# Kernel optimization log

Hardware: AMD Instinct MI355X
Metric: run time of the kernel (lower is better)

## Reference

```python
import jax, jax.numpy as jnp
import numpy as np

NB = 5  # frequency bands


def _ln(x, g, b, eps=1e-5):
    m = jnp.mean(x, axis=-1, keepdims=True)
    v = jnp.var(x, axis=-1, keepdims=True)
    return (x - m) / jnp.sqrt(v + eps) * g + b


def _graph_adj(x, adj_w, sw1, sb1, sw2, sb2, pos_factor, pos_enc):
    # x: [B, D, N] -> degree-normalized adjacency [B, N, N]
    d = x.shape[1]
    xt = jnp.swapaxes(x, 1, 2)  # [B, N, D]
    # concat-MLP first layer split: cat(xi, xj) @ W1 == xi @ W1[:d] + xj @ W1[d:]
    a = xt @ sw1[:d]
    bpart = xt @ sw1[d:]
    h = jax.nn.elu(a[:, :, None, :] + bpart[:, None, :, :] + sb1)  # [B, N, N, H]
    dyn = jax.nn.sigmoid(jnp.squeeze(h @ sw2, -1) + sb2)  # [B, N, N]
    static = jax.nn.softmax(adj_w, axis=-1)
    pos = jax.nn.softmax(pos_enc, axis=-1)
    comb = jax.nn.softmax(static + dyn + pos_factor * pos, axis=-1)
    deg = jnp.sum(comb, axis=-1)
    dis = (deg + 1e-8) ** -0.5
    return dis[:, :, None] * comb * dis[:, None, :]


def _gcn(x, adj, w, b):
    # x: [B, D, N], adj: [B, N, N] -> [B, D_out, N]
    xt = jnp.swapaxes(x, 1, 2)
    out = jnp.einsum('bij,bjd->bid', adj, xt) @ w + b
    return jnp.swapaxes(out, 1, 2)


def _mha(x, qkv_w, qkv_b, ow, ob, nh=4):
    B, S, D = x.shape
    dh = D // nh
    q, k, v = jnp.split(x @ qkv_w + qkv_b, 3, axis=-1)
    q = q.reshape(B, S, nh, dh)
    k = k.reshape(B, S, nh, dh)
    v = v.reshape(B, S, nh, dh)
    att = jax.nn.softmax(jnp.einsum('bihd,bjhd->bhij', q, k) / float(np.sqrt(dh)), axis=-1)
    o = jnp.einsum('bhij,bjhd->bihd', att, v).reshape(B, S, D)
    return o @ ow + ob


def setup_inputs():
    key = jax.random.key(0)
    B, D, N = 16, 256, 64
    ks = iter(jax.random.split(key, 40))

    def rn(shape, s=0.05):
        return jax.random.normal(next(ks), shape, dtype=jnp.float32) * s

    eyeN = jnp.eye(N, dtype=jnp.float32)
    return dict(
        feature=jax.random.normal(next(ks), (B, NB * D, 1, N), dtype=jnp.float32),
        l_adj_w=jnp.tile(eyeN[None], (NB, 1, 1)),
        l_sim_w1=rn((NB, 2 * D, D)), l_sim_b1=jnp.zeros((NB, D), jnp.float32),
        l_sim_w2=rn((NB, D, 1)), l_sim_b2=jnp.zeros((NB, 1), jnp.float32),
        l_pos_factor=jnp.full((NB,), 0.5, jnp.float32),
        l_pos_enc=jnp.tile(eyeN[None], (NB, 1, 1)),
        l_gcn_w=rn((NB, D, D)), l_gcn_b=jnp.zeros((NB, D), jnp.float32),
        g_adj_w=jnp.eye(NB, dtype=jnp.float32),
        g_sim_w1=rn((2 * D, D)), g_sim_b1=jnp.zeros((D,), jnp.float32),
        g_sim_w2=rn((D, 1)), g_sim_b2=jnp.zeros((1,), jnp.float32),
        g_pos_factor=jnp.float32(0.5),
        g_pos_enc=jnp.eye(NB, dtype=jnp.float32),
        g_gcn_w=rn((D, D)), g_gcn_b=jnp.zeros((D,), jnp.float32),
        qkv_w=rn((D, 3 * D)), qkv_b=jnp.zeros((3 * D,), jnp.float32),
        attn_ow=rn((D, D)), attn_ob=jnp.zeros((D,), jnp.float32),
        ln1_g=jnp.ones((D,), jnp.float32), ln1_b=jnp.zeros((D,), jnp.float32),
        ln2_g=jnp.ones((D,), jnp.float32), ln2_b=jnp.zeros((D,), jnp.float32),
        mlp_w1=rn((D, 4 * D)), mlp_b1=jnp.zeros((4 * D,), jnp.float32),
        mlp_w2=rn((4 * D, D)), mlp_b2=jnp.zeros((D,), jnp.float32),
        imp_w=rn((NB, N, 1)), imp_b=jnp.zeros((NB, 1), jnp.float32),
    )


def reference(feature, l_adj_w, l_sim_w1, l_sim_b1, l_sim_w2, l_sim_b2,
              l_pos_factor, l_pos_enc, l_gcn_w, l_gcn_b,
              g_adj_w, g_sim_w1, g_sim_b1, g_sim_w2, g_sim_b2,
              g_pos_factor, g_pos_enc, g_gcn_w, g_gcn_b,
              qkv_w, qkv_b, attn_ow, attn_ob,
              ln1_g, ln1_b, ln2_g, ln2_b,
              mlp_w1, mlp_b1, mlp_w2, mlp_b2,
              imp_w, imp_b):
    B = feature.shape[0]
    D = l_gcn_w.shape[-1]
    N = feature.shape[-1]
    # [B, 5*D, 1, N] -> [5, B, D, N] band-major
    x5 = jnp.moveaxis(feature.reshape(B, NB, D, N), 1, 0)
    # per-band local graphs + GCNs (vmapped over the 5 bands)
    local_adj = jax.vmap(_graph_adj)(x5, l_adj_w, l_sim_w1, l_sim_b1,
                                     l_sim_w2, l_sim_b2, l_pos_factor, l_pos_enc)
    local_out = jax.vmap(_gcn)(x5, local_adj, l_gcn_w, l_gcn_b)  # [5, B, D, N]
    scale_nodes = jnp.moveaxis(jnp.mean(local_out, axis=-1), 0, 1)  # [B, 5, D]
    # cross-band attention block (pre: MHA + residual + LN, then MLP + residual + LN)
    attn = _mha(scale_nodes, qkv_w, qkv_b, attn_ow, attn_ob)
    h1 = _ln(scale_nodes + attn, ln1_g, ln1_b)
    mlp = jax.nn.gelu(h1 @ mlp_w1 + mlp_b1, approximate=False) @ mlp_w2 + mlp_b2
    se = _ln(h1 + mlp, ln2_g, ln2_b)  # [B, 5, D]
    # global scale graph over the 5 band nodes
    xg = jnp.swapaxes(se, 1, 2)  # [B, D, 5]
    g_adj = _graph_adj(xg, g_adj_w, g_sim_w1, g_sim_b1, g_sim_w2, g_sim_b2,
                       g_pos_factor, g_pos_enc)
    g_out = jnp.swapaxes(_gcn(xg, g_adj, g_gcn_w, g_gcn_b), 1, 2)  # [B, 5, D]
    # modulate each local band feature by its global scale vector
    enh = local_out * jnp.moveaxis(g_out, 1, 0)[..., None]  # [5, B, D, N]
    # per-band importance projection over channels: [5, B, D, 1]
    out5 = jnp.einsum('kbdn,kno->kbdo', enh, imp_w) + imp_b[:, None, None, :]
    output = jnp.moveaxis(out5, 0, 1).reshape(B, NB * D, 1, 1)
    return output, g_adj, jnp.moveaxis(local_out, 0, 1)
```

## Files before the change

kernel.cpp:

```cpp
#include <hip/hip_runtime.h>
#include <hip/hip_bf16.h>

#define NBANDS 5
#define BATCH  16
#define DIM    256
#define NNODE  64
#define SEQ    5
#define NHEAD  4
#define DHEAD  64

typedef __hip_bfloat16 bf16;
typedef unsigned short ushort_t;
typedef __attribute__((ext_vector_type(8))) short short8;
typedef __attribute__((ext_vector_type(4))) float float4v;

__device__ __forceinline__ float bu2f(ushort_t u){
    bf16 h = *reinterpret_cast<bf16*>(&u);
    return __bfloat162float(h);
}
__device__ __forceinline__ ushort_t f2bu(float x){
    bf16 h = __float2bfloat16(x);
    return *reinterpret_cast<ushort_t*>(&h);
}

__global__ void __launch_bounds__(256) k_head(
    const float* __restrict__ l_adj_w, const float* __restrict__ l_pos_enc,
    const float* __restrict__ l_pf,
    const float* __restrict__ g_adj_w, const float* __restrict__ g_pos_enc,
    const float* __restrict__ g_pf,
    float* __restrict__ sbase, float* __restrict__ gbase,
    const float* __restrict__ w1, const float* __restrict__ gw,
    ushort_t* __restrict__ w1bt, ushort_t* __restrict__ gwbt,
    const float* __restrict__ feat,
    ushort_t* __restrict__ xtb, ushort_t* __restrict__ xtT)
{
    int blk = blockIdx.x;
    int tid = threadIdx.x;
    __shared__ ushort_t tile[64][65];

    if (blk < 80) {
        int r = blk*4 + (tid>>6);
        int k = r >> 6, i = r & 63;
        int t = tid & 63;
        float aw = l_adj_w[(k*NNODE + i)*NNODE + t];
        float pe = l_pos_enc[(k*NNODE + i)*NNODE + t];
        float m1 = aw, m2 = pe;
        for (int o=32;o>0;o>>=1){ m1 = fmaxf(m1, __shfl_xor(m1,o,64)); m2 = fmaxf(m2, __shfl_xor(m2,o,64)); }
        float e1 = __expf(aw-m1), e2 = __expf(pe-m2);
        float s1=e1, s2=e2;
        for (int o=32;o>0;o>>=1){ s1 += __shfl_xor(s1,o,64); s2 += __shfl_xor(s2,o,64); }
        float pf = l_pf[k];
        sbase[(k*NNODE+i)*NNODE + t] = e1/s1 + pf*(e2/s2);
    } else if (blk == 80) {
        if (tid < NBANDS) {
            int i = tid;
            float r1[NBANDS], r2[NBANDS];
            float m1=-1e30f, m2=-1e30f;
            for (int j=0;j<NBANDS;j++){
                r1[j]=g_adj_w[i*NBANDS+j]; r2[j]=g_pos_enc[i*NBANDS+j];
                m1=fmaxf(m1,r1[j]); m2=fmaxf(m2,r2[j]);
            }
            float s1=0.f,s2=0.f;
            for (int j=0;j<NBANDS;j++){ r1[j]=__expf(r1[j]-m1); r2[j]=__expf(r2[j]-m2); s1+=r1[j]; s2+=r2[j]; }
            float pf = g_pf[0];
            for (int j=0;j<NBANDS;j++) gbase[i*NBANDS+j] = r1[j]/s1 + pf*(r2[j]/s2);
        }
    } else if (blk < 321) {
        int idx = blk - 81;
        int inst = idx >> 4;
        int t = idx & 15;
        int r0 = (t>>2)*64, c0 = (t&3)*64;
        const float* src; ushort_t* dst;
        if (inst < 10){
            int k = inst>>1, half = inst&1;
            src = w1  + ((size_t)k*512 + half*256)*256;
            dst = w1bt+ ((size_t)k*512 + half*256)*256;
        } else {
            int k = inst-10;
            src = gw  + (size_t)k*65536;
            dst = gwbt+ (size_t)k*65536;
        }
        int jj = tid & 63, i4 = tid >> 6;
        for (int p=0;p<16;p++){
            int i = p*4 + i4;
            tile[i][jj] = f2bu(src[(size_t)(r0+i)*256 + c0 + jj]);
        }
        __syncthreads();
        for (int p=0;p<16;p++){
            int i = p*4 + i4;
            dst[(size_t)(c0+i)*256 + r0 + jj] = tile[jj][i];
        }
    } else {
        int idx = blk - 321;
        int k = idx >> 6;
        int b = (idx >> 2) & 15;
        int dt = idx & 3;
        const float* src = feat + ((size_t)b*NBANDS*DIM + (size_t)k*DIM)*NNODE;
        ushort_t* dst = xtb + (size_t)(k*BATCH+b)*NNODE*DIM;
        ushort_t* dstT = xtT + (size_t)(k*BATCH+b)*DIM*NNODE;
        for (int u=0; u<16; ++u){
            int i = dt*4096 + u*256 + tid;
            dstT[i] = f2bu(src[i]);
        }
        for (int r=0;r<16;r++){
            int dp = r*4 + (tid>>6);
            int n  = tid & 63;
            tile[dp][n] = f2bu(src[(size_t)(dt*64+dp)*NNODE + n]);
        }
        __syncthreads();
        for (int r=0;r<16;r++){
            int n  = r*4 + (tid>>6);
            int dp = tid & 63;
            dst[(size_t)n*DIM + dt*64 + dp] = tile[dp][n];
        }
    }
}

__global__ void __launch_bounds__(256) k_ab_mfma(const ushort_t* __restrict__ xtb,
                        const ushort_t* __restrict__ w1bt, const float* __restrict__ b1,
                        ushort_t* __restrict__ aab, ushort_t* __restrict__ bbb)
{
    int blk = blockIdx.x;
    int kband = blk / (BATCH*8);
    int b = (blk/8) % BATCH;
    int nblk = blk & 7;
    int tid = threadIdx.x;
    int wave = tid>>6, lane = tid&63;
    int c16 = lane & 15, quad = lane >> 4;
    int m0 = wave*16;
    size_t rowbase = (size_t)(kband*BATCH+b)*NNODE;
    const ushort_t* Aptr = xtb + (rowbase + m0 + c16)*DIM + quad*8;
    const ushort_t* Bbase = w1bt + (size_t)kband*512*DIM;
    int ncol0 = nblk*64;
    const ushort_t* Bptr0 = Bbase + (size_t)(ncol0 +  0 + c16)*DIM + quad*8;
    const ushort_t* Bptr1 = Bbase + (size_t)(ncol0 + 16 + c16)*DIM + quad*8;
    const ushort_t* Bptr2 = Bbase + (size_t)(ncol0 + 32 + c16)*DIM + quad*8;
    const ushort_t* Bptr3 = Bbase + (size_t)(ncol0 + 48 + c16)*DIM + quad*8;
    float4v acc0 = {0.f,0.f,0.f,0.f}, acc1 = acc0, acc2 = acc0, acc3 = acc0;
    #pragma unroll
    for (int ks=0; ks<8; ++ks){
        short8 a  = *reinterpret_cast<const short8*>(Aptr  + ks*32);
        short8 b0 = *reinterpret_cast<const short8*>(Bptr0 + ks*32);
        short8 b1v= *reinterpret_cast<const short8*>(Bptr1 + ks*32);
        short8 b2 = *reinterpret_cast<const short8*>(Bptr2 + ks*32);
        short8 b3 = *reinterpret_cast<const short8*>(Bptr3 + ks*32);
        acc0 = __builtin_amdgcn_mfma_f32_16x16x32_bf16(a, b0, acc0, 0,0,0);
        acc1 = __builtin_amdgcn_mfma_f32_16x16x32_bf16(a, b1v, acc1, 0,0,0);
        acc2 = __builtin_amdgcn_mfma_f32_16x16x32_bf16(a, b2, acc2, 0,0,0);
        acc3 = __builtin_amdgcn_mfma_f32_16x16x32_bf16(a, b3, acc3, 0,0,0);
    }
    int half = nblk >> 2;
    int cbase = (nblk & 3)*64;
    ushort_t* dst = half ? bbb : aab;
    float4v accs[4] = {acc0, acc1, acc2, acc3};
    #pragma unroll
    for (int nt=0; nt<4; ++nt){
        int cg = cbase + nt*16 + c16;
        float bias = half ? 0.f : b1[kband*DIM + cg];
        #pragma unroll
        for (int r=0;r<4;r++){
            int m = m0 + quad*4 + r;
            dst[(rowbase + m)*DIM + cg] = f2bu(accs[nt][r] + bias);
        }
    }
}

__global__ void __launch_bounds__(256) k_dyn_comb(const ushort_t* __restrict__ aab,
                           const ushort_t* __restrict__ bbb,
                           const float* __restrict__ w2, const float* __restrict__ b2arr,
                           const float* __restrict__ sbase,
                           ushort_t* __restrict__ combb)
{
    int blk = blockIdx.x;
    int k = blk / (BATCH*16);
    int b = (blk / 16) % BATCH;
    int i0 = (blk % 16) * 4;
    int kb = k*BATCH + b;
    __shared__ ushort_t bs[64][260];
    __shared__ float arows[4][DIM];
    __shared__ float w2s[DIM];
    int tid = threadIdx.x;
    int wave = tid >> 6, lane = tid & 63;
    const ushort_t* bsrc = bbb + (size_t)kb*NNODE*DIM;
    for (int u=0; u<16; ++u){
        int idx = u*1024 + tid*4;
        int row = idx >> 8, col = idx & 255;
        *reinterpret_cast<ushort4*>(&bs[row][col]) =
            *reinterpret_cast<const ushort4*>(&bsrc[(size_t)row*DIM + col]);
    }
    for (int r=0;r<4;r++) arows[r][tid] = bu2f(aab[((size_t)kb*NNODE + i0 + r)*DIM + tid]);
    w2s[tid] = w2[k*DIM + tid];
    __syncthreads();

    int i = i0 + wave;
    float acc = 0.f;
    #pragma unroll 4
    for (int dd=0; dd<64; ++dd){
        ushort4 bv = *reinterpret_cast<const ushort4*>(&bs[lane][dd*4]);
        float4 av = *reinterpret_cast<const float4*>(&arows[wave][dd*4]);
        float4 wv = *reinterpret_cast<const float4*>(&w2s[dd*4]);
        float v0 = av.x + bu2f(bv.x);
        float v1 = av.y + bu2f(bv.y);
        float v2 = av.z + bu2f(bv.z);
        float v3 = av.w + bu2f(bv.w);
        float e0 = (v0>0.f)? v0 : (__expf(v0)-1.f);
        float e1 = (v1>0.f)? v1 : (__expf(v1)-1.f);
        float e2 = (v2>0.f)? v2 : (__expf(v2)-1.f);
        float e3 = (v3>0.f)? v3 : (__expf(v3)-1.f);
        acc += e0*wv.x + e1*wv.y + e2*wv.z + e3*wv.w;
    }
    float sb2 = b2arr[k];
    float sg = 1.f/(1.f + __expf(-(acc + sb2)));
    float val = sbase[(k*NNODE + i)*NNODE + lane] + sg;
    float m = val;
    for (int o=32;o>0;o>>=1) m = fmaxf(m, __shfl_xor(m,o,64));
    float e = __expf(val - m);
    float s = e;
    for (int o=32;o>0;o>>=1) s += __shfl_xor(s,o,64);
    combb[((size_t)kb*NNODE + i)*NNODE + lane] = f2bu(e/s);
}

__global__ void __launch_bounds__(256) k_y_mfma(const ushort_t* __restrict__ combb,
                       const ushort_t* __restrict__ xtT,
                       ushort_t* __restrict__ yb)
{
    int blk = blockIdx.x;
    int kband = blk / (BATCH*4);
    int b = (blk/4) % BATCH;
    int nblk = blk & 3;
    int tid = threadIdx.x;
    int wave = tid>>6, lane = tid&63;
    int c16 = lane & 15, quad = lane >> 4;
    int m0 = wave*16;
    int kb = kband*BATCH + b;
    const ushort_t* Aptr = combb + ((size_t)kb*NNODE + m0 + c16)*NNODE + quad*8;
    const ushort_t* Bbase = xtT + (size_t)kb*DIM*NNODE;
    int ncol0 = nblk*64;
    const ushort_t* Bptr0 = Bbase + (size_t)(ncol0 +  0 + c16)*NNODE + quad*8;
    const ushort_t* Bptr1 = Bbase + (size_t)(ncol0 + 16 + c16)*NNODE + quad*8;
    const ushort_t* Bptr2 = Bbase + (size_t)(ncol0 + 32 + c16)*NNODE + quad*8;
    const ushort_t* Bptr3 = Bbase + (size_t)(ncol0 + 48 + c16)*NNODE + quad*8;
    float4v acc0 = {0.f,0.f,0.f,0.f}, acc1 = acc0, acc2 = acc0, acc3 = acc0;
    #pragma unroll
    for (int ks=0; ks<2; ++ks){
        short8 a  = *reinterpret_cast<const short8*>(Aptr  + ks*32);
        short8 b0 = *reinterpret_cast<const short8*>(Bptr0 + ks*32);
        short8 b1v= *reinterpret_cast<const short8*>(Bptr1 + ks*32);
        short8 b2 = *reinterpret_cast<const short8*>(Bptr2 + ks*32);
        short8 b3 = *reinterpret_cast<const short8*>(Bptr3 + ks*32);
        acc0 = __builtin_amdgcn_mfma_f32_16x16x32_bf16(a, b0, acc0, 0,0,0);
        acc1 = __builtin_amdgcn_mfma_f32_16x16x32_bf16(a, b1v, acc1, 0,0,0);
        acc2 = __builtin_amdgcn_mfma_f32_16x16x32_bf16(a, b2, acc2, 0,0,0);
        acc3 = __builtin_amdgcn_mfma_f32_16x16x32_bf16(a, b3, acc3, 0,0,0);
    }
    size_t rowbase = (size_t)kb*NNODE;
    float4v accs[4] = {acc0, acc1, acc2, acc3};
    #pragma unroll
    for (int nt=0; nt<4; ++nt){
        int cg = ncol0 + nt*16 + c16;
        #pragma unroll
        for (int r=0;r<4;r++){
            int m = m0 + quad*4 + r;
            yb[(rowbase + m)*DIM + cg] = f2bu(accs[nt][r]);
        }
    }
}

__global__ void __launch_bounds__(256) k_gcn_mfma(const ushort_t* __restrict__ yb,
                         const ushort_t* __restrict__ gwbt, const float* __restrict__ gb,
                         const float* __restrict__ imp_w,
                         float* __restrict__ out_local,
                         float* __restrict__ scalew, float* __restrict__ impw)
{
    int blk = blockIdx.x;
    int kband = blk / (BATCH*4);
    int b = (blk/4) % BATCH;
    int nblk = blk & 3;
    int tid = threadIdx.x;
    int wave = tid>>6, lane = tid&63;
    int c16 = lane & 15, quad = lane >> 4;
    int m0 = wave*16;
    int kb = kband*BATCH + b;
    __shared__ float iw_s[NNODE];
    __shared__ float sred[4][64];
    __shared__ float ired[4][64];
    if (tid < NNODE) iw_s[tid] = imp_w[kband*NNODE + tid];
    const ushort_t* Aptr = yb + ((size_t)kb*NNODE + m0 + c16)*DIM + quad*8;
    const ushort_t* Bbase = gwbt + (size_t)kband*DIM*DIM;
    int ncol0 = nblk*64;
    const ushort_t* Bptr0 = Bbase + (size_t)(ncol0 +  0 + c16)*DIM + quad*8;
    const ushort_t* Bptr1 = Bbase + (size_t)(ncol0 + 16 + c16)*DIM + quad*8;
    const ushort_t* Bptr2 = Bbase + (size_t)(ncol0 + 32 + c16)*DIM + quad*8;
    const ushort_t* Bptr3 = Bbase + (size_t)(ncol0 + 48 + c16)*DIM + quad*8;
    float4v acc0 = {0.f,0.f,0.f,0.f}, acc1 = acc0, acc2 = acc0, acc3 = acc0;
    #pragma unroll
    for (int ks=0; ks<8; ++ks){
        short8 a  = *reinterpret_cast<const short8*>(Aptr  + ks*32);
        short8 b0 = *reinterpret_cast<const short8*>(Bptr0 + ks*32);
        short8 b1v= *reinterpret_cast<const short8*>(Bptr1 + ks*32);
        short8 b2 = *reinterpret_cast<const short8*>(Bptr2 + ks*32);
        short8 b3 = *reinterpret_cast<const short8*>(Bptr3 + ks*32);
        acc0 = __builtin_amdgcn_mfma_f32_16x16x32_bf16(a, b0, acc0, 0,0,0);
        acc1 = __builtin_amdgcn_mfma_f32_16x16x32_bf16(a, b1v, acc1, 0,0,0);
        acc2 = __builtin_amdgcn_mfma_f32_16x16x32_bf16(a, b2, acc2, 0,0,0);
        acc3 = __builtin_amdgcn_mfma_f32_16x16x32_bf16(a, b3, acc3, 0,0,0);
    }
    __syncthreads();
    float4v accs[4] = {acc0, acc1, acc2, acc3};
    #pragma unroll
    for (int nt=0; nt<4; ++nt){
        int cg = ncol0 + nt*16 + c16;
        float bias = gb[kband*DIM + cg];
        float v0 = accs[nt][0]+bias, v1 = accs[nt][1]+bias, v2 = accs[nt][2]+bias, v3 = accs[nt][3]+bias;
        float4 v = make_float4(v0, v1, v2, v3);
        float* dst = out_local + ((size_t)(b*NBANDS + kband)*DIM + cg)*NNODE + m0 + quad*4;
        *reinterpret_cast<float4*>(dst) = v;
        int nb = m0 + quad*4;
        float s  = v0 + v1 + v2 + v3;
        float di = v0*iw_s[nb] + v1*iw_s[nb+1] + v2*iw_s[nb+2] + v3*iw_s[nb+3];
        s  += __shfl_xor(s, 16, 64);  s  += __shfl_xor(s, 32, 64);
        di += __shfl_xor(di, 16, 64); di += __shfl_xor(di, 32, 64);
        if (quad == 0){
            sred[wave][nt*16 + c16] = s;
            ired[wave][nt*16 + c16] = di;
        }
    }
    __syncthreads();
    if (tid < 64){
        float s  = sred[0][tid] + sred[1][tid] + sred[2][tid] + sred[3][tid];
        float di = ired[0][tid] + ired[1][tid] + ired[2][tid] + ired[3][tid];
        size_t o = ((size_t)b*SEQ + kband)*DIM + ncol0 + tid;
        scalew[o] = s * (1.f/64.f);
        impw[o]   = di;
    }
}

template<int COLS, int SLICES>
__global__ void __launch_bounds__(256) k_gemv(const float* __restrict__ x, const float* __restrict__ w,
                       const float* __restrict__ bias, float* __restrict__ out,
                       int K, int N, int act)
{
    int chunks = N / COLS;
    int row = blockIdx.x / chunks;
    int n0 = (blockIdx.x % chunks) * COLS;
    int c = threadIdx.x % COLS, s = threadIdx.x / COLS;
    __shared__ float xs[1024];
    __shared__ float part[SLICES][COLS];
    for (int i = threadIdx.x; i < K; i += 256) xs[i] = x[(size_t)row*K + i];
    __syncthreads();
    int klen = K / SLICES;
    const float* wp = w + (size_t)(s*klen)*N + n0 + c;
    const float* xp = xs + s*klen;
    float acc = 0.f;
    #pragma unroll 8
    for (int i = 0; i < klen; ++i) acc += xp[i] * wp[(size_t)i*N];
    part[s][c] = acc;
    __syncthreads();
    if (s == 0){
        float v = bias[n0+c];
        #pragma unroll
        for (int q=0;q<SLICES;q++) v += part[q][c];
        if (act) v = 0.5f*v*(1.f + erff(v*0.70710678118654752f));
        out[(size_t)row*N + n0 + c] = v;
    }
}

__global__ void __launch_bounds__(256) k_projattn(const float* __restrict__ qkvw,
                        const float* __restrict__ ow, const float* __restrict__ ob,
                        float* __restrict__ projw)
{
    int row = blockIdx.x / 4;
    int n0 = (blockIdx.x % 4) * 64;
    int b = row / SEQ, i = row % SEQ;
    int tid = threadIdx.x;
    int h = tid >> 6, l = tid & 63;
    __shared__ float xs[DIM];
    __shared__ float part[4][64];
    const float* base = qkvw + (size_t)b*SEQ*3*DIM;
    float qv = base[(size_t)i*3*DIM + h*DHEAD + l];
    float pj[SEQ];
    #pragma unroll
    for (int j=0;j<SEQ;j++){
        float p = qv * base[(size_t)j*3*DIM + DIM + h*DHEAD + l];
        for (int o=32;o>0;o>>=1) p += __shfl_xor(p,o,64);
        pj[j] = p * 0.125f;
    }
    float m = pj[0];
    #pragma unroll
    for (int j=1;j<SEQ;j++) m = fmaxf(m, pj[j]);
    float ssum = 0.f;
    #pragma unroll
    for (int j=0;j<SEQ;j++){ pj[j] = __expf(pj[j]-m); ssum += pj[j]; }
    float inv = 1.f/ssum;
    float o = 0.f;
    #pragma unroll
    for (int j=0;j<SEQ;j++) o += pj[j]*inv * base[(size_t)j*3*DIM + 2*DIM + h*DHEAD + l];
    xs[tid] = o;
    __syncthreads();
    int c = tid & 63, s = tid >> 6;
    const float* wp = ow + (size_t)(s*64)*DIM + n0 + c;
    const float* xp = xs + s*64;
    float acc = 0.f;
    #pragma unroll 8
    for (int k=0;k<64;++k) acc += xp[k] * wp[(size_t)k*DIM];
    part[s][c] = acc;
    __syncthreads();
    if (s == 0){
        projw[(size_t)row*DIM + n0 + c] = ob[n0+c] + part[0][c]+part[1][c]+part[2][c]+part[3][c];
    }
}

__device__ __forceinline__ float block_ln(float v, int tid, float* red, float g, float bln)
{
    float s = v;
    for (int o=32;o>0;o>>=1) s += __shfl_xor(s,o,64);
    int wave = tid>>6, lane = tid&63;
    if (lane==0) red[wave] = s;
    __syncthreads();
    float mean = (red[0]+red[1]+red[2]+red[3]) * (1.f/DIM);
    float c = v - mean;
    float q = c*c;
    for (int o=32;o>0;o>>=1) q += __shfl_xor(q,o,64);
    __syncthreads();
    if (lane==0) red[wave] = q;
    __syncthreads();
    float var = (red[0]+red[1]+red[2]+red[3]) * (1.f/DIM);
    return c * rsqrtf(var + 1e-5f) * g + bln;
}

__global__ void __launch_bounds__(256) k_mlp1_ln(const float* __restrict__ projw,
                         const float* __restrict__ scalew,
                         const float* __restrict__ ln1_g, const float* __restrict__ ln1_b,
                         const float* __restrict__ w1, const float* __restrict__ b1,
                         float* __restrict__ h1w, float* __restrict__ mhw)
{
    int row = blockIdx.x / 16;
    int n0 = (blockIdx.x % 16) * 64;
    int tid = threadIdx.x;
    __shared__ float xs[DIM];
    __shared__ float red[4];
    __shared__ float part[4][64];
    float v = projw[(size_t)row*DIM + tid] + scalew[(size_t)row*DIM + tid];
    float h = block_ln(v, tid, red, ln1_g[tid], ln1_b[tid]);
    xs[tid] = h;
    if ((blockIdx.x % 16) == 0) h1w[(size_t)row*DIM + tid] = h;
    __syncthreads();
    int c = tid & 63, s = tid >> 6;
    const float* wp = w1 + (size_t)(s*64)*1024 + n0 + c;
    const float* xp = xs + s*64;
    float acc = 0.f;
    #pragma unroll 8
    for (int i=0;i<64;++i) acc += xp[i] * wp[(size_t)i*1024];
    part[s][c] = acc;
    __syncthreads();
    if (s == 0){
        float o = b1[n0+c] + part[0][c] + part[1][c] + part[2][c] + part[3][c];
        o = 0.5f*o*(1.f + erff(o*0.70710678118654752f));
        mhw[(size_t)row*1024 + n0 + c] = o;
    }
}

__global__ void __launch_bounds__(256) k_gab_ln(const float* __restrict__ m2w,
                        const float* __restrict__ h1w,
                        const float* __restrict__ ln2_g, const float* __restrict__ ln2_b,
                        const float* __restrict__ gw1, const float* __restrict__ gb1,
                        float* __restrict__ sew, float* __restrict__ gaw, float* __restrict__ gbw)
{
    int row = blockIdx.x / 4;
    int n0 = (blockIdx.x % 4) * 64;
    int tid = threadIdx.x;
    __shared__ float xs[DIM];
    __shared__ float red[4];
    __shared__ float partA[4][64];
    __shared__ float partB[4][64];
    float v = m2w[(size_t)row*DIM + tid] + h1w[(size_t)row*DIM + tid];
    float h = block_ln(v, tid, red, ln2_g[tid], ln2_b[tid]);
    xs[tid] = h;
    if ((blockIdx.x % 4) == 0) sew[(size_t)row*DIM + tid] = h;
    __syncthreads();
    int c = tid & 63, s = tid >> 6;
    const float* wpA = gw1 + (size_t)(s*64)*DIM + n0 + c;
    const float* wpB = wpA + (size_t)DIM*DIM;
    const float* xp = xs + s*64;
    float aA = 0.f, aB = 0.f;
    #pragma unroll 8
    for (int i=0;i<64;++i){
        float xv = xp[i];
        aA += xv * wpA[(size_t)i*DIM];
        aB += xv * wpB[(size_t)i*DIM];
    }
    partA[s][c] = aA;
    partB[s][c] = aB;
    __syncthreads();
    if (s == 0){
        gaw[(size_t)row*DIM + n0 + c] = gb1[n0+c] + partA[0][c]+partA[1][c]+partA[2][c]+partA[3][c];
        gbw[(size_t)row*DIM + n0 + c] = partB[0][c]+partB[1][c]+partB[2][c]+partB[3][c];
    }
}

__global__ void __launch_bounds__(256) k_goutfin(const float* __restrict__ gaw,
                        const float* __restrict__ gbw,
                        const float* __restrict__ gw2, const float* __restrict__ gb2,
                        const float* __restrict__ gbase,
                        const float* __restrict__ sew,
                        const float* __restrict__ ggw, const float* __restrict__ ggb,
                        const float* __restrict__ impw, const float* __restrict__ imp_b,
                        float* __restrict__ out0, float* __restrict__ out_gadj)
{
    int row = blockIdx.x / 4;
    int n0 = (blockIdx.x % 4) * 64;
    int b = row / SEQ, i = row % SEQ;
    int tid = threadIdx.x;
    int wave = tid >> 6, lane = tid & 63;
    __shared__ float dyn_s[SEQ];
    __shared__ float xs[DIM];
    __shared__ float part[4][64];
    for (int j = wave; j < SEQ; j += 4){
        const float* gar = gaw + (size_t)row*DIM;
        const float* gbr = gbw + ((size_t)b*SEQ + j)*DIM;
        float acc = 0.f;
        #pragma unroll
        for (int m=0;m<4;m++){
            int dd = lane + m*64;
            float v = gar[dd] + gbr[dd];
            float e = (v>0.f) ? v : (__expf(v)-1.f);
            acc += e * gw2[dd];
        }
        for (int o=32;o>0;o>>=1) acc += __shfl_xor(acc,o,64);
        if (lane==0) dyn_s[j] = acc;
    }
    __syncthreads();
    float gc[SEQ];
    {
        float sb2 = gb2[0];
        float m = -1e30f;
        #pragma unroll
        for (int j=0;j<SEQ;j++){
            float sg = 1.f/(1.f+__expf(-(dyn_s[j]+sb2)));
            gc[j] = gbase[i*SEQ+j] + sg;
            m = fmaxf(m, gc[j]);
        }
        float ssum=0.f;
        #pragma unroll
        for (int j=0;j<SEQ;j++){ gc[j]=__expf(gc[j]-m); ssum+=gc[j]; }
        float inv = 1.f/ssum;
        #pragma unroll
        for (int j=0;j<SEQ;j++) gc[j] *= inv;
    }
    if (n0 == 0 && tid < SEQ) out_gadj[((size_t)b*SEQ+i)*SEQ + tid] = gc[tid];
    float t = 0.f;
    #pragma unroll
    for (int j=0;j<SEQ;j++) t += gc[j]*sew[((size_t)b*SEQ + j)*DIM + tid];
    xs[tid] = t;
    __syncthreads();
    int c = tid & 63, s = tid >> 6;
    const float* wp = ggw + (size_t)(s*64)*DIM + n0 + c;
    const float* xp = xs + s*64;
    float acc = 0.f;
    #pragma unroll 8
    for (int k=0;k<64;++k) acc += xp[k] * wp[(size_t)k*DIM];
    part[s][c] = acc;
    __syncthreads();
    if (s == 0){
        float g = ggb[n0+c] + part[0][c]+part[1][c]+part[2][c]+part[3][c];
        size_t o = (size_t)row*DIM + n0 + c;
        out0[o] = g * impw[o] + imp_b[i];
    }
}

extern "C" void kernel_launch(void* const* d_in, const int* in_sizes, int n_in,
                              void* d_out, int out_size, void* d_ws, size_t ws_size,
                              hipStream_t stream)
{
    const float* feature      = (const float*)d_in[0];
    const float* l_adj_w      = (const float*)d_in[1];
    const float* l_sim_w1     = (const float*)d_in[2];
    const float* l_sim_b1     = (const float*)d_in[3];
    const float* l_sim_w2     = (const float*)d_in[4];
    const float* l_sim_b2     = (const float*)d_in[5];
    const float* l_pos_factor = (const float*)d_in[6];
    const float* l_pos_enc    = (const float*)d_in[7];
    const float* l_gcn_w      = (const float*)d_in[8];
    const float* l_gcn_b      = (const float*)d_in[9];
    const float* g_adj_w      = (const float*)d_in[10];
    const float* g_sim_w1     = (const float*)d_in[11];
    const float* g_sim_b1     = (const float*)d_in[12];
    const float* g_sim_w2     = (const float*)d_in[13];
    const float* g_sim_b2     = (const float*)d_in[14];
    const float* g_pos_factor = (const float*)d_in[15];
    const float* g_pos_enc    = (const float*)d_in[16];
    const float* g_gcn_w      = (const float*)d_in[17];
    const float* g_gcn_b      = (const float*)d_in[18];
    const float* qkv_w        = (const float*)d_in[19];
    const float* qkv_b        = (const float*)d_in[20];
    const float* attn_ow      = (const float*)d_in[21];
    const float* attn_ob      = (const float*)d_in[22];
    const float* ln1_g        = (const float*)d_in[23];
    const float* ln1_b        = (const float*)d_in[24];
    const float* ln2_g        = (const float*)d_in[25];
    const float* ln2_b        = (const float*)d_in[26];
    const float* mlp_w1       = (const float*)d_in[27];
    const float* mlp_b1       = (const float*)d_in[28];
    const float* mlp_w2       = (const float*)d_in[29];
    const float* mlp_b2       = (const float*)d_in[30];
    const float* imp_w        = (const float*)d_in[31];
    const float* imp_b        = (const float*)d_in[32];

    float* out0      = (float*)d_out;
    float* out_gadj  = out0 + (size_t)BATCH*NBANDS*DIM;
    float* out_local = out_gadj + (size_t)BATCH*NBANDS*NBANDS;

    const size_t BIG = (size_t)NBANDS*BATCH*NNODE*DIM;
    ushort_t* xtb   = (ushort_t*)d_ws;
    ushort_t* aab   = xtb + BIG;
    ushort_t* bbb   = aab + BIG;
    ushort_t* xtT   = bbb + BIG;
    ushort_t* yb    = aab;
    ushort_t* w1bt  = xtT + BIG;
    ushort_t* gwbt  = w1bt + (size_t)NBANDS*512*DIM;
    ushort_t* combb = gwbt + (size_t)NBANDS*DIM*DIM;
    float* fp = (float*)(combb + (size_t)NBANDS*BATCH*NNODE*NNODE);
    float* sbase  = fp; fp += NBANDS*NNODE*NNODE;
    float* gbase  = fp; fp += 32;
    float* scalew = fp; fp += BATCH*SEQ*DIM;
    float* impw   = fp; fp += BATCH*SEQ*DIM;
    float* qkvw   = fp; fp += BATCH*SEQ*3*DIM;
    float* projw  = fp; fp += BATCH*SEQ*DIM;
    float* h1w    = fp; fp += BATCH*SEQ*DIM;
    float* mhw    = fp; fp += BATCH*SEQ*4*DIM;
    float* m2w    = fp; fp += BATCH*SEQ*DIM;
    float* sew    = fp; fp += BATCH*SEQ*DIM;
    float* gaw    = fp; fp += BATCH*SEQ*DIM;
    float* gbw    = fp; fp += BATCH*SEQ*DIM;

    const int ROWS = BATCH*SEQ;

    k_head<<<641, 256, 0, stream>>>(l_adj_w, l_pos_enc, l_pos_factor,
                                    g_adj_w, g_pos_enc, g_pos_factor,
                                    sbase, gbase,
                                    l_sim_w1, l_gcn_w, w1bt, gwbt,
                                    feature, xtb, xtT);
    k_ab_mfma<<<NBANDS*BATCH*8, 256, 0, stream>>>(xtb, w1bt, l_sim_b1, aab, bbb);
    k_dyn_comb<<<NBANDS*BATCH*16, 256, 0, stream>>>(aab, bbb, l_sim_w2, l_sim_b2, sbase, combb);
    k_y_mfma<<<NBANDS*BATCH*4, 256, 0, stream>>>(combb, xtT, yb);
    k_gcn_mfma<<<NBANDS*BATCH*4, 256, 0, stream>>>(yb, gwbt, l_gcn_b, imp_w,
                                                   out_local, scalew, impw);
    k_gemv<64,4><<<ROWS*12, 256, 0, stream>>>(scalew, qkv_w, qkv_b, qkvw, 256, 768, 0);
    k_projattn<<<ROWS*4, 256, 0, stream>>>(qkvw, attn_ow, attn_ob, projw);
    k_mlp1_ln<<<ROWS*16, 256, 0, stream>>>(projw, scalew, ln1_g, ln1_b, mlp_w1, mlp_b1, h1w, mhw);
    k_gemv<32,8><<<ROWS*8, 256, 0, stream>>>(mhw, mlp_w2, mlp_b2, m2w, 1024, 256, 0);
    k_gab_ln<<<ROWS*4, 256, 0, stream>>>(m2w, h1w, ln2_g, ln2_b, g_sim_w1, g_sim_b1, sew, gaw, gbw);
    k_goutfin<<<ROWS*4, 256, 0, stream>>>(gaw, gbw, g_sim_w2, g_sim_b2, gbase,
                                          sew, g_gcn_w, g_gcn_b, impw, imp_b,
                                          out0, out_gadj);
}
```

Before: 218.8 us.

## Fuse local graph pipeline into one kernel and tail into per-batch kernel

Replaces the chain of local-graph kernels (feature transpose, A/B projection, dynamic adjacency, Y, GCN) with one kernel per (band, batch, 16-row quarter) that keeps features, projections, adjacency rows and Y in shared memory. The six small attention/MLP/global-graph kernels become a single 1024-thread kernel per batch. This removes many launches and the large bf16 intermediate round-trips through global memory. In exchange, each block recomputes the full B projection for all 64 nodes (four times redundantly across quarters), and the tail runs on only 16 blocks, so parallelism in the tail is low.

```diff
diff --git a/kernel.cpp b/kernel.cpp
--- a/kernel.cpp
+++ b/kernel.cpp
@@ -6,14 +6,14 @@
 #define DIM    256
 #define NNODE  64
 #define SEQ    5
-#define NHEAD  4
-#define DHEAD  64
 
 typedef __hip_bfloat16 bf16;
 typedef unsigned short ushort_t;
 typedef __attribute__((ext_vector_type(8))) short short8;
 typedef __attribute__((ext_vector_type(4))) float float4v;
 
+#define MFMA __builtin_amdgcn_mfma_f32_16x16x32_bf16
+
 __device__ __forceinline__ float bu2f(ushort_t u){
     bf16 h = *reinterpret_cast<bf16*>(&u);
     return __bfloat162float(h);
@@ -21,6 +21,9 @@
 __device__ __forceinline__ ushort_t f2bu(float x){
     bf16 h = __float2bfloat16(x);
     return *reinterpret_cast<ushort_t*>(&h);
+}
+__device__ __forceinline__ float elu(float v){
+    return (v > 0.f) ? v : (__expf(v) - 1.f);
 }
 
 __global__ void __launch_bounds__(256) k_head(
@@ -30,9 +33,7 @@
     const float* __restrict__ g_pf,
     float* __restrict__ sbase, float* __restrict__ gbase,
     const float* __restrict__ w1, const float* __restrict__ gw,
-    ushort_t* __restrict__ w1bt, ushort_t* __restrict__ gwbt,
-    const float* __restrict__ feat,
-    ushort_t* __restrict__ xtb, ushort_t* __restrict__ xtT)
+    ushort_t* __restrict__ w1bt, ushort_t* __restrict__ gwbt)
 {
     int blk = blockIdx.x;
     int tid = threadIdx.x;
@@ -65,7 +66,7 @@
             float pf = g_pf[0];
             for (int j=0;j<NBANDS;j++) gbase[i*NBANDS+j] = r1[j]/s1 + pf*(r2[j]/s2);
         }
-    } else if (blk < 321) {
+    } else {
         int idx = blk - 81;
         int inst = idx >> 4;
         int t = idx & 15;
@@ -90,481 +91,483 @@
             int i = p*4 + i4;
             dst[(size_t)(c0+i)*256 + r0 + jj] = tile[jj][i];
         }
-    } else {
-        int idx = blk - 321;
-        int k = idx >> 6;
-        int b = (idx >> 2) & 15;
-        int dt = idx & 3;
-        const float* src = feat + ((size_t)b*NBANDS*DIM + (size_t)k*DIM)*NNODE;
-        ushort_t* dst = xtb + (size_t)(k*BATCH+b)*NNODE*DIM;
-        ushort_t* dstT = xtT + (size_t)(k*BATCH+b)*DIM*NNODE;
-        for (int u=0; u<16; ++u){
-            int i = dt*4096 + u*256 + tid;
-            dstT[i] = f2bu(src[i]);
-        }
-        for (int r=0;r<16;r++){
-            int dp = r*4 + (tid>>6);
-            int n  = tid & 63;
-            tile[dp][n] = f2bu(src[(size_t)(dt*64+dp)*NNODE + n]);
-        }
-        __syncthreads();
-        for (int r=0;r<16;r++){
-            int n  = r*4 + (tid>>6);
-            int dp = tid & 63;
-            dst[(size_t)n*DIM + dt*64 + dp] = tile[dp][n];
-        }
-    }
-}
-
-__global__ void __launch_bounds__(256) k_ab_mfma(const ushort_t* __restrict__ xtb,
-                        const ushort_t* __restrict__ w1bt, const float* __restrict__ b1,
-                        ushort_t* __restrict__ aab, ushort_t* __restrict__ bbb)
+    }
+}
+
+__global__ void __launch_bounds__(512) k_graph(
+    const float* __restrict__ feat,
+    const ushort_t* __restrict__ w1bt, const float* __restrict__ b1,
+    const float* __restrict__ w2, const float* __restrict__ b2arr,
+    const float* __restrict__ sbase,
+    const ushort_t* __restrict__ gwbt, const float* __restrict__ gb,
+    const float* __restrict__ imp_w,
+    float* __restrict__ out_local,
+    float* __restrict__ scalew4, float* __restrict__ impw4)
 {
-    int blk = blockIdx.x;
-    int kband = blk / (BATCH*8);
-    int b = (blk/8) % BATCH;
-    int nblk = blk & 7;
+    int k  = blockIdx.x >> 6;
+    int b  = (blockIdx.x >> 2) & 15;
+    int iq = blockIdx.x & 3;
+    int i0 = iq << 4;
     int tid = threadIdx.x;
-    int wave = tid>>6, lane = tid&63;
-    int c16 = lane & 15, quad = lane >> 4;
-    int m0 = wave*16;
-    size_t rowbase = (size_t)(kband*BATCH+b)*NNODE;
-    const ushort_t* Aptr = xtb + (rowbase + m0 + c16)*DIM + quad*8;
-    const ushort_t* Bbase = w1bt + (size_t)kband*512*DIM;
-    int ncol0 = nblk*64;
-    const ushort_t* Bptr0 = Bbase + (size_t)(ncol0 +  0 + c16)*DIM + quad*8;
-    const ushort_t* Bptr1 = Bbase + (size_t)(ncol0 + 16 + c16)*DIM + quad*8;
-    const ushort_t* Bptr2 = Bbase + (size_t)(ncol0 + 32 + c16)*DIM + quad*8;
-    const ushort_t* Bptr3 = Bbase + (size_t)(ncol0 + 48 + c16)*DIM + quad*8;
-    float4v acc0 = {0.f,0.f,0.f,0.f}, acc1 = acc0, acc2 = acc0, acc3 = acc0;
+    int w = tid >> 6, lane = tid & 63, c16 = lane & 15, quad = lane >> 4;
+
+    __shared__ union {
+        ushort_t xtb[64][264];
+        ushort_t ab[80][264];
+    } U;
+    __shared__ ushort_t cs[16][72];
+    __shared__ ushort_t ys[16][264];
+    __shared__ float w2s[DIM];
+
+    const float* src = feat + ((size_t)b*NBANDS + k)*DIM*NNODE;
+
+    if (tid < DIM) w2s[tid] = w2[k*DIM + tid];
     #pragma unroll
-    for (int ks=0; ks<8; ++ks){
-        short8 a  = *reinterpret_cast<const short8*>(Aptr  + ks*32);
-        short8 b0 = *reinterpret_cast<const short8*>(Bptr0 + ks*32);
-        short8 b1v= *reinterpret_cast<const short8*>(Bptr1 + ks*32);
-        short8 b2 = *reinterpret_cast<const short8*>(Bptr2 + ks*32);
-        short8 b3 = *reinterpret_cast<const short8*>(Bptr3 + ks*32);
-        acc0 = __builtin_amdgcn_mfma_f32_16x16x32_bf16(a, b0, acc0, 0,0,0);
-        acc1 = __builtin_amdgcn_mfma_f32_16x16x32_bf16(a, b1v, acc1, 0,0,0);
-        acc2 = __builtin_amdgcn_mfma_f32_16x16x32_bf16(a, b2, acc2, 0,0,0);
-        acc3 = __builtin_amdgcn_mfma_f32_16x16x32_bf16(a, b3, acc3, 0,0,0);
-    }
-    int half = nblk >> 2;
-    int cbase = (nblk & 3)*64;
-    ushort_t* dst = half ? bbb : aab;
-    float4v accs[4] = {acc0, acc1, acc2, acc3};
+    for (int u = 0; u < 32; ++u){
+        int idx = u*512 + tid;
+        U.xtb[idx & 63][idx >> 6] = f2bu(src[idx]);
+    }
+    __syncthreads();
+
+    int col0 = w*32 + c16;
+    int col1 = col0 + 16;
+
+    const ushort_t* Ba = w1bt + (size_t)k*512*DIM;
+    const ushort_t* Bb = Ba + 256*DIM;
+    float4v z = {0.f,0.f,0.f,0.f};
+    float4v aA0=z, aA1=z;
+    float4v aB00=z,aB01=z,aB10=z,aB11=z,aB20=z,aB21=z,aB30=z,aB31=z;
     #pragma unroll
-    for (int nt=0; nt<4; ++nt){
-        int cg = cbase + nt*16 + c16;
-        float bias = half ? 0.f : b1[kband*DIM + cg];
-        #pragma unroll
-        for (int r=0;r<4;r++){
-            int m = m0 + quad*4 + r;
-            dst[(rowbase + m)*DIM + cg] = f2bu(accs[nt][r] + bias);
-        }
-    }
-}
-
-__global__ void __launch_bounds__(256) k_dyn_comb(const ushort_t* __restrict__ aab,
-                           const ushort_t* __restrict__ bbb,
-                           const float* __restrict__ w2, const float* __restrict__ b2arr,
-                           const float* __restrict__ sbase,
-                           ushort_t* __restrict__ combb)
+    for (int ks = 0; ks < 8; ++ks){
+        int ko = ks*32 + quad*8;
+        short8 fa = *reinterpret_cast<const short8*>(&U.xtb[i0 + c16][ko]);
+        short8 f0 = *reinterpret_cast<const short8*>(&U.xtb[ 0 + c16][ko]);
+        short8 f1 = *reinterpret_cast<const short8*>(&U.xtb[16 + c16][ko]);
+        short8 f2 = *reinterpret_cast<const short8*>(&U.xtb[32 + c16][ko]);
+        short8 f3 = *reinterpret_cast<const short8*>(&U.xtb[48 + c16][ko]);
+        short8 wa0 = *reinterpret_cast<const short8*>(Ba + (size_t)col0*DIM + ko);
+        short8 wa1 = *reinterpret_cast<const short8*>(Ba + (size_t)col1*DIM + ko);
+        short8 wb0 = *reinterpret_cast<const short8*>(Bb + (size_t)col0*DIM + ko);
+        short8 wb1 = *reinterpret_cast<const short8*>(Bb + (size_t)col1*DIM + ko);
+        aA0  = MFMA(fa, wa0, aA0, 0,0,0);
+        aA1  = MFMA(fa, wa1, aA1, 0,0,0);
+        aB00 = MFMA(f0, wb0, aB00, 0,0,0);
+        aB01 = MFMA(f0, wb1, aB01, 0,0,0);
+        aB10 = MFMA(f1, wb0, aB10, 0,0,0);
+        aB11 = MFMA(f1, wb1, aB11, 0,0,0);
+        aB20 = MFMA(f2, wb0, aB20, 0,0,0);
+        aB21 = MFMA(f2, wb1, aB21, 0,0,0);
+        aB30 = MFMA(f3, wb0, aB30, 0,0,0);
+        aB31 = MFMA(f3, wb1, aB31, 0,0,0);
+    }
+    __syncthreads();
+    {
+        float bias0 = b1[k*DIM + col0];
+        float bias1 = b1[k*DIM + col1];
+        int r0 = quad*4;
+        #pragma unroll
+        for (int r = 0; r < 4; ++r){
+            U.ab[r0 + r][col0]      = f2bu(aA0[r] + bias0);
+            U.ab[r0 + r][col1]      = f2bu(aA1[r] + bias1);
+            U.ab[16 + r0 + r][col0] = f2bu(aB00[r]);
+            U.ab[16 + r0 + r][col1] = f2bu(aB01[r]);
+            U.ab[32 + r0 + r][col0] = f2bu(aB10[r]);
+            U.ab[32 + r0 + r][col1] = f2bu(aB11[r]);
+            U.ab[48 + r0 + r][col0] = f2bu(aB20[r]);
+            U.ab[48 + r0 + r][col1] = f2bu(aB21[r]);
+            U.ab[64 + r0 + r][col0] = f2bu(aB30[r]);
+            U.ab[64 + r0 + r][col1] = f2bu(aB31[r]);
+        }
+    }
+    __syncthreads();
+
+    {
+        int il0 = w*2, il1 = w*2 + 1;
+        float acc0 = 0.f, acc1 = 0.f;
+        const ushort_t* ar0 = U.ab[il0];
+        const ushort_t* ar1 = U.ab[il1];
+        const ushort_t* br  = U.ab[16 + lane];
+        #pragma unroll 4
+        for (int dd = 0; dd < 64; ++dd){
+            ushort4 bv = *reinterpret_cast<const ushort4*>(br  + dd*4);
+            ushort4 a0 = *reinterpret_cast<const ushort4*>(ar0 + dd*4);
+            ushort4 a1 = *reinterpret_cast<const ushort4*>(ar1 + dd*4);
+            float4 wv  = *reinterpret_cast<const float4*>(&w2s[dd*4]);
+            float bx = bu2f(bv.x), by = bu2f(bv.y), bz = bu2f(bv.z), bq = bu2f(bv.w);
+            acc0 += elu(bu2f(a0.x)+bx)*wv.x + elu(bu2f(a0.y)+by)*wv.y
+                  + elu(bu2f(a0.z)+bz)*wv.z + elu(bu2f(a0.w)+bq)*wv.w;
+            acc1 += elu(bu2f(a1.x)+bx)*wv.x + elu(bu2f(a1.y)+by)*wv.y
+                  + elu(bu2f(a1.z)+bz)*wv.z + elu(bu2f(a1.w)+bq)*wv.w;
+        }
+        float sb2 = b2arr[k];
+        float sg0 = 1.f/(1.f + __expf(-(acc0 + sb2)));
+        float sg1 = 1.f/(1.f + __expf(-(acc1 + sb2)));
+        float val0 = sbase[(k*NNODE + i0 + il0)*NNODE + lane] + sg0;
+        float val1 = sbase[(k*NNODE + i0 + il1)*NNODE + lane] + sg1;
+        float m0 = val0, m1 = val1;
+        for (int o=32;o>0;o>>=1){ m0 = fmaxf(m0, __shfl_xor(m0,o,64)); m1 = fmaxf(m1, __shfl_xor(m1,o,64)); }
+        float e0 = __expf(val0 - m0), e1 = __expf(val1 - m1);
+        float s0 = e0, s1 = e1;
+        for (int o=32;o>0;o>>=1){ s0 += __shfl_xor(s0,o,64); s1 += __shfl_xor(s1,o,64); }
+        cs[il0][lane] = f2bu(e0/s0);
+        cs[il1][lane] = f2bu(e1/s1);
+    }
+    __syncthreads();
+
+    {
+        float4v aY0 = z, aY1 = z;
+        #pragma unroll
+        for (int ks = 0; ks < 2; ++ks){
+            int ko = ks*32 + quad*8;
+            short8 af = *reinterpret_cast<const short8*>(&cs[c16][ko]);
+            const float* f0p = src + (size_t)col0*NNODE + ko;
+            const float* f1p = src + (size_t)col1*NNODE + ko;
+            float4 x0 = *reinterpret_cast<const float4*>(f0p);
+            float4 x1 = *reinterpret_cast<const float4*>(f0p+4);
+            float4 y0 = *reinterpret_cast<const float4*>(f1p);
+            float4 y1 = *reinterpret_cast<const float4*>(f1p+4);
+            short8 bf0, bf1;
+            bf0[0]=(short)f2bu(x0.x); bf0[1]=(short)f2bu(x0.y); bf0[2]=(short)f2bu(x0.z); bf0[3]=(short)f2bu(x0.w);
+            bf0[4]=(short)f2bu(x1.x); bf0[5]=(short)f2bu(x1.y); bf0[6]=(short)f2bu(x1.z); bf0[7]=(short)f2bu(x1.w);
+            bf1[0]=(short)f2bu(y0.x); bf1[1]=(short)f2bu(y0.y); bf1[2]=(short)f2bu(y0.z); bf1[3]=(short)f2bu(y0.w);
+            bf1[4]=(short)f2bu(y1.x); bf1[5]=(short)f2bu(y1.y); bf1[6]=(short)f2bu(y1.z); bf1[7]=(short)f2bu(y1.w);
+            aY0 = MFMA(af, bf0, aY0, 0,0,0);
+            aY1 = MFMA(af, bf1, aY1, 0,0,0);
+        }
+        #pragma unroll
+        for (int r=0;r<4;++r){
+            ys[quad*4 + r][col0] = f2bu(aY0[r]);
+            ys[quad*4 + r][col1] = f2bu(aY1[r]);
+        }
+    }
+    __syncthreads();
+
+    {
+        float4v aG0 = z, aG1 = z;
+        const ushort_t* Bg = gwbt + (size_t)k*DIM*DIM;
+        #pragma unroll
+        for (int ks = 0; ks < 8; ++ks){
+            int ko = ks*32 + quad*8;
+            short8 af = *reinterpret_cast<const short8*>(&ys[c16][ko]);
+            short8 g0 = *reinterpret_cast<const short8*>(Bg + (size_t)col0*DIM + ko);
+            short8 g1 = *reinterpret_cast<const short8*>(Bg + (size_t)col1*DIM + ko);
+            aG0 = MFMA(af, g0, aG0, 0,0,0);
+            aG1 = MFMA(af, g1, aG1, 0,0,0);
+        }
+        int nb = i0 + quad*4;
+        float iw0 = imp_w[k*NNODE + nb + 0];
+        float iw1 = imp_w[k*NNODE + nb + 1];
+        float iw2 = imp_w[k*NNODE + nb + 2];
+        float iw3 = imp_w[k*NNODE + nb + 3];
+        size_t obase = ((size_t)b*NBANDS + k)*DIM;
+
+        float bias0 = gb[k*DIM + col0];
+        float v0 = aG0[0]+bias0, v1 = aG0[1]+bias0, v2 = aG0[2]+bias0, v3 = aG0[3]+bias0;
+        float4 vv = make_float4(v0,v1,v2,v3);
+        *reinterpret_cast<float4*>(&out_local[(obase + col0)*NNODE + nb]) = vv;
+        float s  = v0+v1+v2+v3;
+        float di = v0*iw0 + v1*iw1 + v2*iw2 + v3*iw3;
+        s  += __shfl_xor(s,16,64);  s  += __shfl_xor(s,32,64);
+        di += __shfl_xor(di,16,64); di += __shfl_xor(di,32,64);
+        if (quad == 0){
+            size_t o = ((size_t)iq*80 + b*SEQ + k)*DIM + col0;
+            scalew4[o] = s;
+            impw4[o]   = di;
+        }
+
+        float bias1 = gb[k*DIM + col1];
+        v0 = aG1[0]+bias1; v1 = aG1[1]+bias1; v2 = aG1[2]+bias1; v3 = aG1[3]+bias1;
+        vv = make_float4(v0,v1,v2,v3);
+        *reinterpret_cast<float4*>(&out_local[(obase + col1)*NNODE + nb]) = vv;
+        s  = v0+v1+v2+v3;
+        di = v0*iw0 + v1*iw1 + v2*iw2 + v3*iw3;
+        s  += __shfl_xor(s,16,64);  s  += __shfl_xor(s,32,64);
+        di += __shfl_xor(di,16,64); di += __shfl_xor(di,32,64);
+        if (quad == 0){
+            size_t o = ((size_t)iq*80 + b*SEQ + k)*DIM + col1;
+            scalew4[o] = s;
+            impw4[o]   = di;
+        }
+    }
+}
+
+__device__ __forceinline__ void ln_row(float* row, const float* g, const float* bb, int lane)
 {
-    int blk = blockIdx.x;
-    int k = blk / (BATCH*16);
-    int b = (blk / 16) % BATCH;
-    int i0 = (blk % 16) * 4;
-    int kb = k*BATCH + b;
-    __shared__ ushort_t bs[64][260];
-    __shared__ float arows[4][DIM];
-    __shared__ float w2s[DIM];
+    float v0 = row[lane], v1 = row[lane+64], v2 = row[lane+128], v3 = row[lane+192];
+    float s = v0+v1+v2+v3;
+    for (int o=32;o>0;o>>=1) s += __shfl_xor(s,o,64);
+    float mean = s * (1.f/256.f);
+    float c0 = v0-mean, c1 = v1-mean, c2 = v2-mean, c3 = v3-mean;
+    float q = c0*c0+c1*c1+c2*c2+c3*c3;
+    for (int o=32;o>0;o>>=1) q += __shfl_xor(q,o,64);
+    float rs = rsqrtf(q*(1.f/256.f) + 1e-5f);
+    row[lane]     = c0*rs*g[lane]     + bb[lane];
+    row[lane+64]  = c1*rs*g[lane+64]  + bb[lane+64];
+    row[lane+128] = c2*rs*g[lane+128] + bb[lane+128];
+    row[lane+192] = c3*rs*g[lane+192] + bb[lane+192];
+}
+
+__global__ void __launch_bounds__(1024) k_tail(
+    const float* __restrict__ scalew4, const float* __restrict__ impw4,
+    const float* __restrict__ qkv_w, const float* __restrict__ qkv_b,
+    const float* __restrict__ attn_ow, const float* __restrict__ attn_ob,
+    const float* __restrict__ ln1_g, const float* __restrict__ ln1_b,
+    const float* __restrict__ mlp_w1, const float* __restrict__ mlp_b1,
+    const float* __restrict__ mlp_w2, const float* __restrict__ mlp_b2,
+    const float* __restrict__ ln2_g, const float* __restrict__ ln2_b,
+    const float* __restrict__ gw1, const float* __restrict__ gb1,
+    const float* __restrict__ gw2, const float* __restrict__ gb2,
+    const float* __restrict__ gbase,
+    const float* __restrict__ ggw, const float* __restrict__ ggb,
+    const float* __restrict__ imp_b,
+    float* __restrict__ out0, float* __restrict__ out_gadj)
+{
+    int b = blockIdx.x;
     int tid = threadIdx.x;
-    int wave = tid >> 6, lane = tid & 63;
-    const ushort_t* bsrc = bbb + (size_t)kb*NNODE*DIM;
-    for (int u=0; u<16; ++u){
-        int idx = u*1024 + tid*4;
-        int row = idx >> 8, col = idx & 255;
-        *reinterpret_cast<ushort4*>(&bs[row][col]) =
-            *reinterpret_cast<const ushort4*>(&bsrc[(size_t)row*DIM + col]);
-    }
-    for (int r=0;r<4;r++) arows[r][tid] = bu2f(aab[((size_t)kb*NNODE + i0 + r)*DIM + tid]);
-    w2s[tid] = w2[k*DIM + tid];
-    __syncthreads();
-
-    int i = i0 + wave;
-    float acc = 0.f;
-    #pragma unroll 4
-    for (int dd=0; dd<64; ++dd){
-        ushort4 bv = *reinterpret_cast<const ushort4*>(&bs[lane][dd*4]);
-        float4 av = *reinterpret_cast<const float4*>(&arows[wave][dd*4]);
-        float4 wv = *reinterpret_cast<const float4*>(&w2s[dd*4]);
-        float v0 = av.x + bu2f(bv.x);
-        float v1 = av.y + bu2f(bv.y);
-        float v2 = av.z + bu2f(bv.z);
-        float v3 = av.w + bu2f(bv.w);
-        float e0 = (v0>0.f)? v0 : (__expf(v0)-1.f);
-        float e1 = (v1>0.f)? v1 : (__expf(v1)-1.f);
-        float e2 = (v2>0.f)? v2 : (__expf(v2)-1.f);
-        float e3 = (v3>0.f)? v3 : (__expf(v3)-1.f);
-        acc += e0*wv.x + e1*wv.y + e2*wv.z + e3*wv.w;
-    }
-    float sb2 = b2arr[k];
-    float sg = 1.f/(1.f + __expf(-(acc + sb2)));
-    float val = sbase[(k*NNODE + i)*NNODE + lane] + sg;
-    float m = val;
-    for (int o=32;o>0;o>>=1) m = fmaxf(m, __shfl_xor(m,o,64));
-    float e = __expf(val - m);
-    float s = e;
-    for (int o=32;o>0;o>>=1) s += __shfl_xor(s,o,64);
-    combb[((size_t)kb*NNODE + i)*NNODE + lane] = f2bu(e/s);
-}
-
-__global__ void __launch_bounds__(256) k_y_mfma(const ushort_t* __restrict__ combb,
-                       const ushort_t* __restrict__ xtT,
-                       ushort_t* __restrict__ yb)
-{
-    int blk = blockIdx.x;
-    int kband = blk / (BATCH*4);
-    int b = (blk/4) % BATCH;
-    int nblk = blk & 3;
-    int tid = threadIdx.x;
-    int wave = tid>>6, lane = tid&63;
-    int c16 = lane & 15, quad = lane >> 4;
-    int m0 = wave*16;
-    int kb = kband*BATCH + b;
-    const ushort_t* Aptr = combb + ((size_t)kb*NNODE + m0 + c16)*NNODE + quad*8;
-    const ushort_t* Bbase = xtT + (size_t)kb*DIM*NNODE;
-    int ncol0 = nblk*64;
-    const ushort_t* Bptr0 = Bbase + (size_t)(ncol0 +  0 + c16)*NNODE + quad*8;
-    const ushort_t* Bptr1 = Bbase + (size_t)(ncol0 + 16 + c16)*NNODE + quad*8;
-    const ushort_t* Bptr2 = Bbase + (size_t)(ncol0 + 32 + c16)*NNODE + quad*8;
-    const ushort_t* Bptr3 = Bbase + (size_t)(ncol0 + 48 + c16)*NNODE + quad*8;
-    float4v acc0 = {0.f,0.f,0.f,0.f}, acc1 = acc0, acc2 = acc0, acc3 = acc0;
+    int w = tid >> 6, lane = tid & 63;
+
+    __shared__ __align__(16) float A[5160];
+    __shared__ __align__(16) float Bp[5200];
+    __shared__ __align__(16) float C[1300];
+    __shared__ __align__(16) float Dx[1300];
+    __shared__ __align__(16) float E[1300];
+    __shared__ float F[64];
+
     #pragma unroll
-    for (int ks=0; ks<2; ++ks){
-        short8 a  = *reinterpret_cast<const short8*>(Aptr  + ks*32);
-        short8 b0 = *reinterpret_cast<const short8*>(Bptr0 + ks*32);
-        short8 b1v= *reinterpret_cast<const short8*>(Bptr1 + ks*32);
-        short8 b2 = *reinterpret_cast<const short8*>(Bptr2 + ks*32);
-        short8 b3 = *reinterpret_cast<const short8*>(Bptr3 + ks*32);
-        acc0 = __builtin_amdgcn_mfma_f32_16x16x32_bf16(a, b0, acc0, 0,0,0);
-        acc1 = __builtin_amdgcn_mfma_f32_16x16x32_bf16(a, b1v, acc1, 0,0,0);
-        acc2 = __builtin_amdgcn_mfma_f32_16x16x32_bf16(a, b2, acc2, 0,0,0);
-        acc3 = __builtin_amdgcn_mfma_f32_16x16x32_bf16(a, b3, acc3, 0,0,0);
-    }
-    size_t rowbase = (size_t)kb*NNODE;
-    float4v accs[4] = {acc0, acc1, acc2, acc3};
-    #pragma unroll
-    for (int nt=0; nt<4; ++nt){
-        int cg = ncol0 + nt*16 + c16;
-        #pragma unroll
-        for (int r=0;r<4;r++){
-            int m = m0 + quad*4 + r;
-            yb[(rowbase + m)*DIM + cg] = f2bu(accs[nt][r]);
-        }
-    }
-}
-
-__global__ void __launch_bounds__(256) k_gcn_mfma(const ushort_t* __restrict__ yb,
-                         const ushort_t* __restrict__ gwbt, const float* __restrict__ gb,
-                         const float* __restrict__ imp_w,
-                         float* __restrict__ out_local,
-                         float* __restrict__ scalew, float* __restrict__ impw)
-{
-    int blk = blockIdx.x;
-    int kband = blk / (BATCH*4);
-    int b = (blk/4) % BATCH;
-    int nblk = blk & 3;
-    int tid = threadIdx.x;
-    int wave = tid>>6, lane = tid&63;
-    int c16 = lane & 15, quad = lane >> 4;
-    int m0 = wave*16;
-    int kb = kband*BATCH + b;
-    __shared__ float iw_s[NNODE];
-    __shared__ float sred[4][64];
-    __shared__ float ired[4][64];
-    if (tid < NNODE) iw_s[tid] = imp_w[kband*NNODE + tid];
-    const ushort_t* Aptr = yb + ((size_t)kb*NNODE + m0 + c16)*DIM + quad*8;
-    const ushort_t* Bbase = gwbt + (size_t)kband*DIM*DIM;
-    int ncol0 = nblk*64;
-    const ushort_t* Bptr0 = Bbase + (size_t)(ncol0 +  0 + c16)*DIM + quad*8;
-    const ushort_t* Bptr1 = Bbase + (size_t)(ncol0 + 16 + c16)*DIM + quad*8;
-    const ushort_t* Bptr2 = Bbase + (size_t)(ncol0 + 32 + c16)*DIM + quad*8;
-    const ushort_t* Bptr3 = Bbase + (size_t)(ncol0 + 48 + c16)*DIM + quad*8;
-    float4v acc0 = {0.f,0.f,0.f,0.f}, acc1 = acc0, acc2 = acc0, acc3 = acc0;
-    #pragma unroll
-    for (int ks=0; ks<8; ++ks){
-        short8 a  = *reinterpret_cast<const short8*>(Aptr  + ks*32);
-        short8 b0 = *reinterpret_cast<const short8*>(Bptr0 + ks*32);
-        short8 b1v= *reinterpret_cast<const short8*>(Bptr1 + ks*32);
-        short8 b2 = *reinterpret_cast<const short8*>(Bptr2 + ks*32);
-        short8 b3 = *reinterpret_cast<const short8*>(Bptr3 + ks*32);
-        acc0 = __builtin_amdgcn_mfma_f32_16x16x32_bf16(a, b0, acc0, 0,0,0);
-        acc1 = __builtin_amdgcn_mfma_f32_16x16x32_bf16(a, b1v, acc1, 0,0,0);
-        acc2 = __builtin_amdgcn_mfma_f32_16x16x32_bf16(a, b2, acc2, 0,0,0);
-        acc3 = __builtin_amdgcn_mfma_f32_16x16x32_bf16(a, b3, acc3, 0,0,0);
-    }
-    __syncthreads();
-    float4v accs[4] = {acc0, acc1, acc2, acc3};
-    #pragma unroll
-    for (int nt=0; nt<4; ++nt){
-        int cg = ncol0 + nt*16 + c16;
-        float bias = gb[kband*DIM + cg];
-        float v0 = accs[nt][0]+bias, v1 = accs[nt][1]+bias, v2 = accs[nt][2]+bias, v3 = accs[nt][3]+bias;
-        float4 v = make_float4(v0, v1, v2, v3);
-        float* dst = out_local + ((size_t)(b*NBANDS + kband)*DIM + cg)*NNODE + m0 + quad*4;
-        *reinterpret_cast<float4*>(dst) = v;
-        int nb = m0 + quad*4;
-        float s  = v0 + v1 + v2 + v3;
-        float di = v0*iw_s[nb] + v1*iw_s[nb+1] + v2*iw_s[nb+2] + v3*iw_s[nb+3];
-        s  += __shfl_xor(s, 16, 64);  s  += __shfl_xor(s, 32, 64);
-        di += __shfl_xor(di, 16, 64); di += __shfl_xor(di, 32, 64);
-        if (quad == 0){
-            sred[wave][nt*16 + c16] = s;
-            ired[wave][nt*16 + c16] = di;
-        }
-    }
-    __syncthreads();
-    if (tid < 64){
-        float s  = sred[0][tid] + sred[1][tid] + sred[2][tid] + sred[3][tid];
-        float di = ired[0][tid] + ired[1][tid] + ired[2][tid] + ired[3][tid];
-        size_t o = ((size_t)b*SEQ + kband)*DIM + ncol0 + tid;
-        scalew[o] = s * (1.f/64.f);
-        impw[o]   = di;
-    }
-}
-
-template<int COLS, int SLICES>
-__global__ void __launch_bounds__(256) k_gemv(const float* __restrict__ x, const float* __restrict__ w,
-                       const float* __restrict__ bias, float* __restrict__ out,
-                       int K, int N, int act)
-{
-    int chunks = N / COLS;
-    int row = blockIdx.x / chunks;
-    int n0 = (blockIdx.x % chunks) * COLS;
-    int c = threadIdx.x % COLS, s = threadIdx.x / COLS;
-    __shared__ float xs[1024];
-    __shared__ float part[SLICES][COLS];
-    for (int i = threadIdx.x; i < K; i += 256) xs[i] = x[(size_t)row*K + i];
-    __syncthreads();
-    int klen = K / SLICES;
-    const float* wp = w + (size_t)(s*klen)*N + n0 + c;
-    const float* xp = xs + s*klen;
-    float acc = 0.f;
-    #pragma unroll 8
-    for (int i = 0; i < klen; ++i) acc += xp[i] * wp[(size_t)i*N];
-    part[s][c] = acc;
-    __syncthreads();
-    if (s == 0){
-        float v = bias[n0+c];
-        #pragma unroll
-        for (int q=0;q<SLICES;q++) v += part[q][c];
-        if (act) v = 0.5f*v*(1.f + erff(v*0.70710678118654752f));
-        out[(size_t)row*N + n0 + c] = v;
-    }
-}
-
-__global__ void __launch_bounds__(256) k_projattn(const float* __restrict__ qkvw,
-                        const float* __restrict__ ow, const float* __restrict__ ob,
-                        float* __restrict__ projw)
-{
-    int row = blockIdx.x / 4;
-    int n0 = (blockIdx.x % 4) * 64;
-    int b = row / SEQ, i = row % SEQ;
-    int tid = threadIdx.x;
-    int h = tid >> 6, l = tid & 63;
-    __shared__ float xs[DIM];
-    __shared__ float part[4][64];
-    const float* base = qkvw + (size_t)b*SEQ*3*DIM;
-    float qv = base[(size_t)i*3*DIM + h*DHEAD + l];
-    float pj[SEQ];
-    #pragma unroll
-    for (int j=0;j<SEQ;j++){
-        float p = qv * base[(size_t)j*3*DIM + DIM + h*DHEAD + l];
-        for (int o=32;o>0;o>>=1) p += __shfl_xor(p,o,64);
-        pj[j] = p * 0.125f;
-    }
-    float m = pj[0];
-    #pragma unroll
-    for (int j=1;j<SEQ;j++) m = fmaxf(m, pj[j]);
-    float ssum = 0.f;
-    #pragma unroll
-    for (int j=0;j<SEQ;j++){ pj[j] = __expf(pj[j]-m); ssum += pj[j]; }
-    float inv = 1.f/ssum;
-    float o = 0.f;
-    #pragma unroll
-    for (int j=0;j<SEQ;j++) o += pj[j]*inv * base[(size_t)j*3*DIM + 2*DIM + h*DHEAD + l];
-    xs[tid] = o;
-    __syncthreads();
-    int c = tid & 63, s = tid >> 6;
-    const float* wp = ow + (size_t)(s*64)*DIM + n0 + c;
-    const float* xp = xs + s*64;
-    float acc = 0.f;
-    #pragma unroll 8
-    for (int k=0;k<64;++k) acc += xp[k] * wp[(size_t)k*DIM];
-    part[s][c] = acc;
-    __syncthreads();
-    if (s == 0){
-        projw[(size_t)row*DIM + n0 + c] = ob[n0+c] + part[0][c]+part[1][c]+part[2][c]+part[3][c];
-    }
-}
-
-__device__ __forceinline__ float block_ln(float v, int tid, float* red, float g, float bln)
-{
-    float s = v;
-    for (int o=32;o>0;o>>=1) s += __shfl_xor(s,o,64);
-    int wave = tid>>6, lane = tid&63;
-    if (lane==0) red[wave] = s;
-    __syncthreads();
-    float mean = (red[0]+red[1]+red[2]+red[3]) * (1.f/DIM);
-    float c = v - mean;
-    float q = c*c;
-    for (int o=32;o>0;o>>=1) q += __shfl_xor(q,o,64);
-    __syncthreads();
-    if (lane==0) red[wave] = q;
-    __syncthreads();
-    float var = (red[0]+red[1]+red[2]+red[3]) * (1.f/DIM);
-    return c * rsqrtf(var + 1e-5f) * g + bln;
-}
-
-__global__ void __launch_bounds__(256) k_mlp1_ln(const float* __restrict__ projw,
-                         const float* __restrict__ scalew,
-                         const float* __restrict__ ln1_g, const float* __restrict__ ln1_b,
-                         const float* __restrict__ w1, const float* __restrict__ b1,
-                         float* __restrict__ h1w, float* __restrict__ mhw)
-{
-    int row = blockIdx.x / 16;
-    int n0 = (blockIdx.x % 16) * 64;
-    int tid = threadIdx.x;
-    __shared__ float xs[DIM];
-    __shared__ float red[4];
-    __shared__ float part[4][64];
-    float v = projw[(size_t)row*DIM + tid] + scalew[(size_t)row*DIM + tid];
-    float h = block_ln(v, tid, red, ln1_g[tid], ln1_b[tid]);
-    xs[tid] = h;
-    if ((blockIdx.x % 16) == 0) h1w[(size_t)row*DIM + tid] = h;
-    __syncthreads();
-    int c = tid & 63, s = tid >> 6;
-    const float* wp = w1 + (size_t)(s*64)*1024 + n0 + c;
-    const float* xp = xs + s*64;
-    float acc = 0.f;
-    #pragma unroll 8
-    for (int i=0;i<64;++i) acc += xp[i] * wp[(size_t)i*1024];
-    part[s][c] = acc;
-    __syncthreads();
-    if (s == 0){
-        float o = b1[n0+c] + part[0][c] + part[1][c] + part[2][c] + part[3][c];
-        o = 0.5f*o*(1.f + erff(o*0.70710678118654752f));
-        mhw[(size_t)row*1024 + n0 + c] = o;
-    }
-}
-
-__global__ void __launch_bounds__(256) k_gab_ln(const float* __restrict__ m2w,
-                        const float* __restrict__ h1w,
-                        const float* __restrict__ ln2_g, const float* __restrict__ ln2_b,
-                        const float* __restrict__ gw1, const float* __restrict__ gb1,
-                        float* __restrict__ sew, float* __restrict__ gaw, float* __restrict__ gbw)
-{
-    int row = blockIdx.x / 4;
-    int n0 = (blockIdx.x % 4) * 64;
-    int tid = threadIdx.x;
-    __shared__ float xs[DIM];
-    __shared__ float red[4];
-    __shared__ float partA[4][64];
-    __shared__ float partB[4][64];
-    float v = m2w[(size_t)row*DIM + tid] + h1w[(size_t)row*DIM + tid];
-    float h = block_ln(v, tid, red, ln2_g[tid], ln2_b[tid]);
-    xs[tid] = h;
-    if ((blockIdx.x % 4) == 0) sew[(size_t)row*DIM + tid] = h;
-    __syncthreads();
-    int c = tid & 63, s = tid >> 6;
-    const float* wpA = gw1 + (size_t)(s*64)*DIM + n0 + c;
-    const float* wpB = wpA + (size_t)DIM*DIM;
-    const float* xp = xs + s*64;
-    float aA = 0.f, aB = 0.f;
-    #pragma unroll 8
-    for (int i=0;i<64;++i){
-        float xv = xp[i];
-        aA += xv * wpA[(size_t)i*DIM];
-        aB += xv * wpB[(size_t)i*DIM];
-    }
-    partA[s][c] = aA;
-    partB[s][c] = aB;
-    __syncthreads();
-    if (s == 0){
-        gaw[(size_t)row*DIM + n0 + c] = gb1[n0+c] + partA[0][c]+partA[1][c]+partA[2][c]+partA[3][c];
-        gbw[(size_t)row*DIM + n0 + c] = partB[0][c]+partB[1][c]+partB[2][c]+partB[3][c];
-    }
-}
-
-__global__ void __launch_bounds__(256) k_goutfin(const float* __restrict__ gaw,
-                        const float* __restrict__ gbw,
-                        const float* __restrict__ gw2, const float* __restrict__ gb2,
-                        const float* __restrict__ gbase,
-                        const float* __restrict__ sew,
-                        const float* __restrict__ ggw, const float* __restrict__ ggb,
-                        const float* __restrict__ impw, const float* __restrict__ imp_b,
-                        float* __restrict__ out0, float* __restrict__ out_gadj)
-{
-    int row = blockIdx.x / 4;
-    int n0 = (blockIdx.x % 4) * 64;
-    int b = row / SEQ, i = row % SEQ;
-    int tid = threadIdx.x;
-    int wave = tid >> 6, lane = tid & 63;
-    __shared__ float dyn_s[SEQ];
-    __shared__ float xs[DIM];
-    __shared__ float part[4][64];
-    for (int j = wave; j < SEQ; j += 4){
-        const float* gar = gaw + (size_t)row*DIM;
-        const float* gbr = gbw + ((size_t)b*SEQ + j)*DIM;
+    for (int p = 0; p < 2; ++p){
+        int id = tid + p*1024;
+        if (id < SEQ*DIM){
+            int i = id >> 8, d = id & 255;
+            size_t base = ((size_t)b*SEQ + i)*DIM + d;
+            float v = scalew4[base] + scalew4[20480 + base]
+                    + scalew4[40960 + base] + scalew4[61440 + base];
+            C[i*260 + d] = v * (1.f/64.f);
+        }
+    }
+    __syncthreads();
+
+    if (tid < 768){
+        int n = tid;
+        float bias = qkv_b[n];
+        float acc[5] = {bias,bias,bias,bias,bias};
+        for (int d = 0; d < DIM; d += 4){
+            float wv0 = qkv_w[(size_t)d*768 + n];
+            float wv1 = qkv_w[(size_t)(d+1)*768 + n];
+            float wv2 = qkv_w[(size_t)(d+2)*768 + n];
+            float wv3 = qkv_w[(size_t)(d+3)*768 + n];
+            #pragma unroll
+            for (int i=0;i<5;++i){
+                float4 cv = *reinterpret_cast<const float4*>(&C[i*260 + d]);
+                acc[i] += cv.x*wv0 + cv.y*wv1 + cv.z*wv2 + cv.w*wv3;
+            }
+        }
+        #pragma unroll
+        for (int i=0;i<5;++i) A[i*772 + n] = acc[i];
+    }
+    __syncthreads();
+
+    for (int p = w; p < 20; p += 16){
+        int i = p >> 2, h = p & 3;
+        float qv = A[i*772 + h*64 + lane];
+        float pj[SEQ];
+        #pragma unroll
+        for (int j=0;j<SEQ;++j){
+            float x = qv * A[j*772 + 256 + h*64 + lane];
+            for (int o=32;o>0;o>>=1) x += __shfl_xor(x,o,64);
+            pj[j] = x * 0.125f;
+        }
+        float m = pj[0];
+        #pragma unroll
+        for (int j=1;j<SEQ;++j) m = fmaxf(m, pj[j]);
+        float ss = 0.f;
+        #pragma unroll
+        for (int j=0;j<SEQ;++j){ pj[j] = __expf(pj[j]-m); ss += pj[j]; }
+        float inv = 1.f/ss;
+        float o = 0.f;
+        #pragma unroll
+        for (int j=0;j<SEQ;++j) o += pj[j]*inv * A[j*772 + 512 + h*64 + lane];
+        Dx[i*260 + h*64 + lane] = o;
+    }
+    __syncthreads();
+
+    if (tid < DIM){
+        int n = tid;
+        float bias = attn_ob[n];
+        float acc[5] = {bias,bias,bias,bias,bias};
+        for (int d = 0; d < DIM; d += 4){
+            float wv0 = attn_ow[(size_t)d*DIM + n];
+            float wv1 = attn_ow[(size_t)(d+1)*DIM + n];
+            float wv2 = attn_ow[(size_t)(d+2)*DIM + n];
+            float wv3 = attn_ow[(size_t)(d+3)*DIM + n];
+            #pragma unroll
+            for (int i=0;i<5;++i){
+                float4 xv = *reinterpret_cast<const float4*>(&Dx[i*260 + d]);
+                acc[i] += xv.x*wv0 + xv.y*wv1 + xv.z*wv2 + xv.w*wv3;
+            }
+        }
+        #pragma unroll
+        for (int i=0;i<5;++i) E[i*260 + n] = C[i*260 + n] + acc[i];
+    }
+    __syncthreads();
+    if (w < SEQ) ln_row(&E[w*260], ln1_g, ln1_b, lane);
+    __syncthreads();
+
+    {
+        int m = tid;
+        float bias = mlp_b1[m];
+        float acc[5] = {bias,bias,bias,bias,bias};
+        for (int d = 0; d < DIM; d += 4){
+            float wv0 = mlp_w1[(size_t)d*1024 + m];
+            float wv1 = mlp_w1[(size_t)(d+1)*1024 + m];
+            float wv2 = mlp_w1[(size_t)(d+2)*1024 + m];
+            float wv3 = mlp_w1[(size_t)(d+3)*1024 + m];
+            #pragma unroll
+            for (int i=0;i<5;++i){
+                float4 xv = *reinterpret_cast<const float4*>(&E[i*260 + d]);
+                acc[i] += xv.x*wv0 + xv.y*wv1 + xv.z*wv2 + xv.w*wv3;
+            }
+        }
+        #pragma unroll
+        for (int i=0;i<5;++i){
+            float v = acc[i];
+            A[i*1032 + m] = 0.5f*v*(1.f + erff(v*0.70710678118654752f));
+        }
+    }
+    __syncthreads();
+
+    {
+        int n = tid & 255, s = tid >> 8;
+        float acc[5] = {0.f,0.f,0.f,0.f,0.f};
+        const float* wbase = mlp_w2 + (size_t)s*256*DIM + n;
+        const float* mbase = A + s*256;
+        for (int kk = 0; kk < 256; kk += 4){
+            float wv0 = wbase[(size_t)kk*DIM];
+            float wv1 = wbase[(size_t)(kk+1)*DIM];
+            float wv2 = wbase[(size_t)(kk+2)*DIM];
+            float wv3 = wbase[(size_t)(kk+3)*DIM];
+            #pragma unroll
+            for (int i=0;i<5;++i){
+                float4 xv = *reinterpret_cast<const float4*>(&mbase[i*1032 + kk]);
+                acc[i] += xv.x*wv0 + xv.y*wv1 + xv.z*wv2 + xv.w*wv3;
+            }
+        }
+        #pragma unroll
+        for (int i=0;i<5;++i) Bp[(s*5 + i)*260 + n] = acc[i];
+    }
+    __syncthreads();
+    if (tid < DIM){
+        int n = tid;
+        float b2v = mlp_b2[n];
+        #pragma unroll
+        for (int i=0;i<5;++i){
+            float m2 = b2v + Bp[i*260+n] + Bp[(5+i)*260+n] + Bp[(10+i)*260+n] + Bp[(15+i)*260+n];
+            C[i*260 + n] = m2 + E[i*260 + n];
+        }
+    }
+    __syncthreads();
+    if (w < SEQ) ln_row(&C[w*260], ln2_g, ln2_b, lane);
+    __syncthreads();
+
+    {
+        int n = tid & 255, s = tid >> 8;
+        int mat = s >> 1, half = s & 1;
+        float acc[5] = {0.f,0.f,0.f,0.f,0.f};
+        const float* wbase = gw1 + ((size_t)mat*DIM + half*128)*DIM + n;
+        for (int kk = 0; kk < 128; kk += 4){
+            int d = half*128 + kk;
+            float wv0 = wbase[(size_t)kk*DIM];
+            float wv1 = wbase[(size_t)(kk+1)*DIM];
+            float wv2 = wbase[(size_t)(kk+2)*DIM];
+            float wv3 = wbase[(size_t)(kk+3)*DIM];
+            #pragma unroll
+            for (int i=0;i<5;++i){
+                float4 xv = *reinterpret_cast<const float4*>(&C[i*260 + d]);
+                acc[i] += xv.x*wv0 + xv.y*wv1 + xv.z*wv2 + xv.w*wv3;
+            }
+        }
+        #pragma unroll
+        for (int i=0;i<5;++i) Bp[(s*5 + i)*260 + n] = acc[i];
+    }
+    __syncthreads();
+    if (tid < DIM){
+        int n = tid;
+        float g1v = gb1[n];
+        #pragma unroll
+        for (int i=0;i<5;++i){
+            A[i*260 + n]        = g1v + Bp[i*260+n] + Bp[(5+i)*260+n];
+            A[1300 + i*260 + n] =       Bp[(10+i)*260+n] + Bp[(15+i)*260+n];
+        }
+    }
+    __syncthreads();
+
+    for (int p = w; p < 25; p += 16){
+        int i = p/5, j = p - (p/5)*5;
         float acc = 0.f;
         #pragma unroll
-        for (int m=0;m<4;m++){
-            int dd = lane + m*64;
-            float v = gar[dd] + gbr[dd];
-            float e = (v>0.f) ? v : (__expf(v)-1.f);
-            acc += e * gw2[dd];
+        for (int q = 0; q < 4; ++q){
+            int d = lane + q*64;
+            float v = A[i*260 + d] + A[1300 + j*260 + d];
+            acc += elu(v) * gw2[d];
         }
         for (int o=32;o>0;o>>=1) acc += __shfl_xor(acc,o,64);
-        if (lane==0) dyn_s[j] = acc;
-    }
-    __syncthreads();
-    float gc[SEQ];
-    {
+        if (lane == 0) F[p] = acc;
+    }
+    __syncthreads();
+    if (tid < SEQ){
+        int i = tid;
         float sb2 = gb2[0];
+        float gc[SEQ];
         float m = -1e30f;
         #pragma unroll
-        for (int j=0;j<SEQ;j++){
-            float sg = 1.f/(1.f+__expf(-(dyn_s[j]+sb2)));
-            gc[j] = gbase[i*SEQ+j] + sg;
+        for (int j=0;j<SEQ;++j){
+            float sg = 1.f/(1.f + __expf(-(F[i*5+j] + sb2)));
+            gc[j] = gbase[i*SEQ + j] + sg;
             m = fmaxf(m, gc[j]);
         }
-        float ssum=0.f;
-        #pragma unroll
-        for (int j=0;j<SEQ;j++){ gc[j]=__expf(gc[j]-m); ssum+=gc[j]; }
-        float inv = 1.f/ssum;
-        #pragma unroll
-        for (int j=0;j<SEQ;j++) gc[j] *= inv;
-    }
-    if (n0 == 0 && tid < SEQ) out_gadj[((size_t)b*SEQ+i)*SEQ + tid] = gc[tid];
-    float t = 0.f;
-    #pragma unroll
-    for (int j=0;j<SEQ;j++) t += gc[j]*sew[((size_t)b*SEQ + j)*DIM + tid];
-    xs[tid] = t;
-    __syncthreads();
-    int c = tid & 63, s = tid >> 6;
-    const float* wp = ggw + (size_t)(s*64)*DIM + n0 + c;
-    const float* xp = xs + s*64;
-    float acc = 0.f;
-    #pragma unroll 8
-    for (int k=0;k<64;++k) acc += xp[k] * wp[(size_t)k*DIM];
-    part[s][c] = acc;
-    __syncthreads();
-    if (s == 0){
-        float g = ggb[n0+c] + part[0][c]+part[1][c]+part[2][c]+part[3][c];
-        size_t o = (size_t)row*DIM + n0 + c;
-        out0[o] = g * impw[o] + imp_b[i];
+        float ss = 0.f;
+        #pragma unroll
+        for (int j=0;j<SEQ;++j){ gc[j] = __expf(gc[j]-m); ss += gc[j]; }
+        float inv = 1.f/ss;
+        #pragma unroll
+        for (int j=0;j<SEQ;++j){
+            float v = gc[j]*inv;
+            F[32 + i*5 + j] = v;
+            out_gadj[((size_t)b*SEQ + i)*SEQ + j] = v;
+        }
+    }
+    __syncthreads();
+    if (tid < DIM){
+        int n = tid;
+        #pragma unroll
+        for (int i=0;i<5;++i){
+            float t = 0.f;
+            #pragma unroll
+            for (int j=0;j<SEQ;++j) t += F[32 + i*5 + j] * C[j*260 + n];
+            Dx[i*260 + n] = t;
+        }
+    }
+    __syncthreads();
+    if (tid < DIM){
+        int n = tid;
+        float bias = ggb[n];
+        float acc[5] = {bias,bias,bias,bias,bias};
+        for (int d = 0; d < DIM; d += 4){
+            float wv0 = ggw[(size_t)d*DIM + n];
+            float wv1 = ggw[(size_t)(d+1)*DIM + n];
+            float wv2 = ggw[(size_t)(d+2)*DIM + n];
+            float wv3 = ggw[(size_t)(d+3)*DIM + n];
+            #pragma unroll
+            for (int i=0;i<5;++i){
+                float4 xv = *reinterpret_cast<const float4*>(&Dx[i*260 + d]);
+                acc[i] += xv.x*wv0 + xv.y*wv1 + xv.z*wv2 + xv.w*wv3;
+            }
+        }
+        #pragma unroll
+        for (int i=0;i<5;++i){
+            size_t rowo = ((size_t)b*SEQ + i)*DIM + n;
+            float imps = impw4[rowo] + impw4[20480 + rowo] + impw4[40960 + rowo] + impw4[61440 + rowo];
+            out0[rowo] = acc[i]*imps + imp_b[i];
+        }
     }
 }
 
@@ -610,47 +613,27 @@
     float* out_gadj  = out0 + (size_t)BATCH*NBANDS*DIM;
     float* out_local = out_gadj + (size_t)BATCH*NBANDS*NBANDS;
 
-    const size_t BIG = (size_t)NBANDS*BATCH*NNODE*DIM;
-    ushort_t* xtb   = (ushort_t*)d_ws;
-    ushort_t* aab   = xtb + BIG;
-    ushort_t* bbb   = aab + BIG;
-    ushort_t* xtT   = bbb + BIG;
-    ushort_t* yb    = aab;
-    ushort_t* w1bt  = xtT + BIG;
-    ushort_t* gwbt  = w1bt + (size_t)NBANDS*512*DIM;
-    ushort_t* combb = gwbt + (size_t)NBANDS*DIM*DIM;
-    float* fp = (float*)(combb + (size_t)NBANDS*BATCH*NNODE*NNODE);
-    float* sbase  = fp; fp += NBANDS*NNODE*NNODE;
-    float* gbase  = fp; fp += 32;
-    float* scalew = fp; fp += BATCH*SEQ*DIM;
-    float* impw   = fp; fp += BATCH*SEQ*DIM;
-    float* qkvw   = fp; fp += BATCH*SEQ*3*DIM;
-    float* projw  = fp; fp += BATCH*SEQ*DIM;
-    float* h1w    = fp; fp += BATCH*SEQ*DIM;
-    float* mhw    = fp; fp += BATCH*SEQ*4*DIM;
-    float* m2w    = fp; fp += BATCH*SEQ*DIM;
-    float* sew    = fp; fp += BATCH*SEQ*DIM;
-    float* gaw    = fp; fp += BATCH*SEQ*DIM;
-    float* gbw    = fp; fp += BATCH*SEQ*DIM;
-
-    const int ROWS = BATCH*SEQ;
-
-    k_head<<<641, 256, 0, stream>>>(l_adj_w, l_pos_enc, l_pos_factor,
+    ushort_t* w1bt = (ushort_t*)d_ws;
+    ushort_t* gwbt = w1bt + (size_t)NBANDS*512*DIM;
+    float* fp = (float*)(gwbt + (size_t)NBANDS*DIM*DIM);
+    float* sbase   = fp; fp += NBANDS*NNODE*NNODE;
+    float* gbase   = fp; fp += 32;
+    float* scalew4 = fp; fp += 4*BATCH*SEQ*DIM;
+    float* impw4   = fp; fp += 4*BATCH*SEQ*DIM;
+
+    k_head<<<321, 256, 0, stream>>>(l_adj_w, l_pos_enc, l_pos_factor,
                                     g_adj_w, g_pos_enc, g_pos_factor,
                                     sbase, gbase,
-                                    l_sim_w1, l_gcn_w, w1bt, gwbt,
-                                    feature, xtb, xtT);
-    k_ab_mfma<<<NBANDS*BATCH*8, 256, 0, stream>>>(xtb, w1bt, l_sim_b1, aab, bbb);
-    k_dyn_comb<<<NBANDS*BATCH*16, 256, 0, stream>>>(aab, bbb, l_sim_w2, l_sim_b2, sbase, combb);
-    k_y_mfma<<<NBANDS*BATCH*4, 256, 0, stream>>>(combb, xtT, yb);
-    k_gcn_mfma<<<NBANDS*BATCH*4, 256, 0, stream>>>(yb, gwbt, l_gcn_b, imp_w,
-                                                   out_local, scalew, impw);
-    k_gemv<64,4><<<ROWS*12, 256, 0, stream>>>(scalew, qkv_w, qkv_b, qkvw, 256, 768, 0);
-    k_projattn<<<ROWS*4, 256, 0, stream>>>(qkvw, attn_ow, attn_ob, projw);
-    k_mlp1_ln<<<ROWS*16, 256, 0, stream>>>(projw, scalew, ln1_g, ln1_b, mlp_w1, mlp_b1, h1w, mhw);
-    k_gemv<32,8><<<ROWS*8, 256, 0, stream>>>(mhw, mlp_w2, mlp_b2, m2w, 1024, 256, 0);
-    k_gab_ln<<<ROWS*4, 256, 0, stream>>>(m2w, h1w, ln2_g, ln2_b, g_sim_w1, g_sim_b1, sew, gaw, gbw);
-    k_goutfin<<<ROWS*4, 256, 0, stream>>>(gaw, gbw, g_sim_w2, g_sim_b2, gbase,
-                                          sew, g_gcn_w, g_gcn_b, impw, imp_b,
-                                          out0, out_gadj);
-}
+                                    l_sim_w1, l_gcn_w, w1bt, gwbt);
+    k_graph<<<NBANDS*BATCH*4, 512, 0, stream>>>(feature, w1bt, l_sim_b1,
+                                    l_sim_w2, l_sim_b2, sbase,
+                                    gwbt, l_gcn_b, imp_w,
+                                    out_local, scalew4, impw4);
+    k_tail<<<BATCH, 1024, 0, stream>>>(scalew4, impw4, qkv_w, qkv_b,
+                                    attn_ow, attn_ob, ln1_g, ln1_b,
+                                    mlp_w1, mlp_b1, mlp_w2, mlp_b2,
+                                    ln2_g, ln2_b, g_sim_w1, g_sim_b1,
+                                    g_sim_w2, g_sim_b2, gbase,
+                                    g_gcn_w, g_gcn_b, imp_b,
+                                    out0, out_gadj);
+}
```

After: 265.0 us. 1.21x slower.
